# Optimization experiments

Hardware: AMD Instinct MI355X
Metric: run time of the kernel (lower is better)

Reference implementation:

```python
import jax, jax.numpy as jnp
import numpy as np
import math

N_HEAD = 16
HEAD_DIM = 64
LN_EPS = 1e-5
TEMP = 1.0

def _layernorm(x, scale, bias):
    # normalize over last dim (head_dim)
    mu = jnp.mean(x, axis=-1, keepdims=True)
    var = jnp.mean(jnp.square(x - mu), axis=-1, keepdims=True)
    return (x - mu) / jnp.sqrt(var + LN_EPS) * scale + bias

def setup_inputs() -> dict:
    key = jax.random.key(0)
    ks = jax.random.split(key, 3)
    B, S, C = 4, 2048, 1024
    x = jax.random.normal(ks[0], (B, S, C), dtype=jnp.float32)
    w_qkv = jax.random.normal(ks[1], (C, 3 * C), dtype=jnp.float32) * (C ** -0.5)
    w_proj = jax.random.normal(ks[2], (C, C), dtype=jnp.float32) * (C ** -0.5)
    return {
        "x": x,
        "w_qkv": w_qkv,
        "w_proj": w_proj,
        "q_scale": jnp.ones((HEAD_DIM,), jnp.float32),
        "q_bias": jnp.zeros((HEAD_DIM,), jnp.float32),
        "k_scale": jnp.ones((HEAD_DIM,), jnp.float32),
        "k_bias": jnp.zeros((HEAD_DIM,), jnp.float32),
    }

def reference(x, w_qkv, w_proj, q_scale, q_bias, k_scale, k_bias):
    B, S, C = x.shape
    H, D = N_HEAD, HEAD_DIM
    # qkv projection -> [B,S,3,H,D] -> [3,B,H,S,D]
    qkv = (x @ w_qkv).reshape(B, S, 3, H, D).transpose(2, 0, 3, 1, 4)
    q = _layernorm(qkv[0], q_scale, q_bias)
    k = _layernorm(qkv[1], k_scale, k_bias)
    v = qkv[2]
    # temperature-scaled logits, stable softmax
    inv = 1.0 / (math.sqrt(D) * max(TEMP, 1e-6))
    logits = jnp.einsum('bhqd,bhkd->bhqk', q, k) * inv
    att = jax.nn.softmax(logits, axis=-1)
    # entropy stats (track_stats=True path)
    s_raw = -jnp.sum(att * jnp.log(att + 1e-9), axis=-1)  # [B,H,S]
    batch_entropies = jnp.mean(s_raw / math.log(S), axis=(1, 2))  # [B]
    out = jnp.einsum('bhqk,bhkd->bhqd', att, v).transpose(0, 2, 1, 3).reshape(B, S, C)
    return out @ w_proj, batch_entropies
```

## Files before the change

### kernel.cpp

```cpp
#include <hip/hip_runtime.h>
#include <hip/hip_bf16.h>
#include <math.h>

#define CB 4
#define CS 2048
#define CC 1024
#define CH 16
#define CD 64
#define CBS (CB*CS)

typedef unsigned short u16;
typedef __bf16 bf16x8 __attribute__((ext_vector_type(8)));
typedef float f32x4 __attribute__((ext_vector_type(4)));
typedef float f32x16 __attribute__((ext_vector_type(16)));
typedef unsigned short u16x4 __attribute__((ext_vector_type(4)));
typedef unsigned short u16x8 __attribute__((ext_vector_type(8)));
typedef unsigned u32x2 __attribute__((ext_vector_type(2)));

__device__ __forceinline__ u16 f2bf(float f){
  union { float f; unsigned u; } v; v.f = f;
  unsigned r = v.u + 0x7FFFu + ((v.u >> 16) & 1u);
  return (u16)(r >> 16);
}
__device__ __forceinline__ unsigned pack2bf(float a, float b){
  __hip_bfloat162 h = __float22bfloat162_rn(make_float2(a, b));
  union { __hip_bfloat162 h; unsigned u; } c; c.h = h; return c.u;
}
__device__ __forceinline__ f32x4 mfma16(bf16x8 a, bf16x8 b, f32x4 c){
  return __builtin_amdgcn_mfma_f32_16x16x32_bf16(a, b, c, 0, 0, 0);
}
__device__ __forceinline__ f32x16 mfma32(bf16x8 a, bf16x8 b, f32x16 c){
  return __builtin_amdgcn_mfma_f32_32x32x16_bf16(a, b, c, 0, 0, 0);
}
__device__ __forceinline__ void gload16(const u16* g, u16* lds_base_uniform){
  __builtin_amdgcn_global_load_lds(
      (const __attribute__((address_space(1))) unsigned int*)g,
      (__attribute__((address_space(3))) unsigned int*)lds_base_uniform, 16, 0, 0);
}

__global__ __launch_bounds__(256) void convert_x_kernel(
    const float* __restrict__ x, u16* __restrict__ xb, float* __restrict__ zero4){
  if (blockIdx.x == 0 && threadIdx.x < 4) zero4[threadIdx.x] = 0.0f;
  size_t i = ((size_t)blockIdx.x*256 + threadIdx.x)*8;
  float4 a = *(const float4*)(x+i);
  float4 b = *(const float4*)(x+i+4);
  u16x8 o = { f2bf(a.x),f2bf(a.y),f2bf(a.z),f2bf(a.w),
              f2bf(b.x),f2bf(b.y),f2bf(b.z),f2bf(b.w) };
  *(u16x8*)(xb+i) = o;
}

template<int K, int N>
__global__ __launch_bounds__(256) void transpose_convert_kernel(
    const float* __restrict__ w, u16* __restrict__ wt){
  __shared__ u16 tile[64][65];
  const int nb = N/64;
  int tk0 = (blockIdx.x / nb) * 64;
  int tn0 = (blockIdx.x % nb) * 64;
  int t = threadIdx.x;
  for (int i = 0; i < 4; i++) {
    int r = i*16 + (t>>4);
    int c = (t&15)*4;
    float4 v = *(const float4*)(w + (size_t)(tk0+r)*N + tn0 + c);
    tile[c+0][r]=f2bf(v.x); tile[c+1][r]=f2bf(v.y);
    tile[c+2][r]=f2bf(v.z); tile[c+3][r]=f2bf(v.w);
  }
  __syncthreads();
  for (int i = 0; i < 4; i++) {
    int r = i*16 + (t>>4);
    int c = (t&15)*4;
    u16x4 o = { tile[r][c+0], tile[r][c+1], tile[r][c+2], tile[r][c+3] };
    *(u16x4*)(wt + (size_t)(tn0+r)*K + tk0 + c) = o;
  }
}

__global__ __launch_bounds__(256) void transpose_v_kernel(
    const u16* __restrict__ vb, u16* __restrict__ vtb){
  __shared__ u16 tile[64][72];
  int bh = blockIdx.x >> 5;
  int st = blockIdx.x & 31;
  int t = threadIdx.x;
  const u16* src = vb + (size_t)bh*CS*CD + (size_t)st*64*CD;
  int r = t>>2, c = (t&3)*16;
  *(u16x8*)&tile[r][c]   = *(const u16x8*)(src + (size_t)r*CD + c);
  *(u16x8*)&tile[r][c+8] = *(const u16x8*)(src + (size_t)r*CD + c + 8);
  __syncthreads();
  int d = t>>2, s = (t&3)*16;
  u16x8 o0, o1;
  for (int j=0;j<8;j++){ o0[j] = tile[s+j][d]; o1[j] = tile[s+8+j][d]; }
  u16* dst = vtb + (size_t)bh*CD*CS + (size_t)d*CS + st*64 + s;
  *(u16x8*)dst = o0;
  *(u16x8*)(dst+8) = o1;
}

__global__ __launch_bounds__(256, 2) void gemm_qkv_ln_kernel(
    const u16* __restrict__ xb, const u16* __restrict__ wqkvT,
    const float* __restrict__ qsc, const float* __restrict__ qbi,
    const float* __restrict__ ksc, const float* __restrict__ kbi,
    u16* __restrict__ qb, u16* __restrict__ kb, u16* __restrict__ vb){
  __shared__ u16 al[128*64];
  __shared__ u16 bl[128*64];
  int t = threadIdx.x;
  int wv = t >> 6, lane = t & 63, lo = lane & 15, q4 = lane >> 4;
  int m0 = blockIdx.x * 128;
  int n0 = blockIdx.y * 128;
  int srow = lane >> 3, scol = (lane & 7) * 8;
  const u16* ag = xb    + (size_t)(m0 + srow)*CC + scol;
  const u16* bg = wqkvT + (size_t)(n0 + srow)*CC + scol;

  f32x4 acc[2][8];
  for (int i=0;i<2;i++) for (int j=0;j<8;j++) acc[i][j] = (f32x4){0.f,0.f,0.f,0.f};

  for (int kk = 0; kk < 16; kk++){
    int k0 = kk * 64;
    for (int i = 0; i < 4; i++){
      int inst = i*4 + wv;
      gload16(ag + (size_t)inst*8*CC + k0, al + inst*512);
      gload16(bg + (size_t)inst*8*CC + k0, bl + inst*512);
    }
    __syncthreads();
    for (int ksI = 0; ksI < 2; ksI++){
      int koff = ksI*32 + q4*8;
      bf16x8 a0 = *(const bf16x8*)&al[(wv*32      + lo)*64 + koff];
      bf16x8 a1 = *(const bf16x8*)&al[(wv*32 + 16 + lo)*64 + koff];
      for (int nt=0; nt<8; nt++){
        bf16x8 b = *(const bf16x8*)&bl[(nt*16 + lo)*64 + koff];
        acc[0][nt] = mfma16(a0, b, acc[0][nt]);
        acc[1][nt] = mfma16(a1, b, acc[1][nt]);
      }
    }
    __syncthreads();
  }

  int three = n0 >> 10;
  int h0 = (n0 & 1023) >> 6;
  const float* scp = (three == 0) ? qsc : ksc;
  const float* bip = (three == 0) ? qbi : kbi;
  float outscale = (three == 0) ? 0.125f * 1.44269504088896f : 1.0f;
  u16* dst = (three == 0) ? qb : (three == 1 ? kb : vb);

  for (int rt = 0; rt < 2; rt++){
    int tg = m0 + wv*32 + rt*16 + q4*4;
    for (int hf = 0; hf < 2; hf++){
      int h = h0 + hf;
      for (int r = 0; r < 4; r++){
        int token = tg + r;
        int bb = token >> 11, ss = token & (CS-1);
        size_t base = (((size_t)(bb*CH + h))*CS + ss)*CD;
        if (three < 2){
          float s1 = 0.f, s2 = 0.f;
          for (int j=0;j<4;j++){ float v = acc[rt][hf*4+j][r]; s1 += v; s2 += v*v; }
          for (int off=8; off>=1; off>>=1){
            s1 += __shfl_xor(s1, off, 16);
            s2 += __shfl_xor(s2, off, 16);
          }
          float mean = s1 * (1.f/64.f);
          float var  = s2 * (1.f/64.f) - mean*mean;
          float rstd = rsqrtf(var + 1e-5f);
          for (int j=0;j<4;j++){
            int d = j*16 + lo;
            float v = (acc[rt][hf*4+j][r] - mean) * rstd * scp[d] + bip[d];
            dst[base + d] = f2bf(v * outscale);
          }
        } else {
          for (int j=0;j<4;j++){
            int d = j*16 + lo;
            dst[base + d] = f2bf(acc[rt][hf*4+j][r]);
          }
        }
      }
    }
  }
}

__global__ __launch_bounds__(256, 4) void attention_kernel(
    const u16* __restrict__ qb, const u16* __restrict__ kb,
    const u16* __restrict__ vtb, u16* __restrict__ attnb, float* __restrict__ ent){
  __shared__ __align__(16) u16 kl[2][64*64];
  __shared__ __align__(16) u16 vl[2][64*64];
  __shared__ __align__(16) float zl[4][32];
  int t = threadIdx.x;
  int wv = t >> 6, lane = t & 63;
  int col = lane & 31, hi = lane >> 5;
  int n = blockIdx.x;
  int xc = n & 7, j = n >> 3;
  int bh = xc + 8*(j >> 4);
  int qt = j & 15;
  int bI = bh >> 4;
  int q0w = qt*128 + wv*32;
  const u16* qbp = qb  + (size_t)bh * CS * CD;
  const u16* kbp = kb  + (size_t)bh * CS * CD;
  const u16* vbp = vtb + (size_t)bh * CD * CS;

  int srow  = lane >> 3;
  int sslot = (lane & 7) ^ srow;

  bf16x8 qf[4];
  for (int ks=0;ks<4;ks++)
    qf[ks] = *(const bf16x8*)(qbp + (size_t)(q0w + col)*CD + ks*16 + hi*8);

  f32x16 o[2];
  for (int nt=0;nt<2;nt++) for (int i=0;i<16;i++) o[nt][i] = 0.f;
  float zacc = 0.f, tacc = 0.f;

  for (int c=0;c<2;c++){
    int chunk = wv*2 + c;
    int row = chunk*8 + srow;
    gload16(kbp + (size_t)row*CD + sslot*8, &kl[0][chunk*512]);
    gload16(vbp + (size_t)row*CS + sslot*8, &vl[0][chunk*512]);
  }

  const int cshift = (col & 7);

  for (int it = 0; it < 32; it++){
    const int cur = it & 1, nxt = cur ^ 1;
    __syncthreads();
    if (it < 31){
      int skn = (it+1)*64;
      for (int c=0;c<2;c++){
        int chunk = wv*2 + c;
        int row = chunk*8 + srow;
        gload16(kbp + (size_t)(skn + row)*CD + sslot*8, &kl[nxt][chunk*512]);
        gload16(vbp + (size_t)row*CS + skn + sslot*8, &vl[nxt][chunk*512]);
      }
    }

    bf16x8 kfr[2][4], vfr[2][4];
    for (int mt=0;mt<2;mt++)
      for (int ks=0;ks<4;ks++)
        kfr[mt][ks] = *(const bf16x8*)&kl[cur][(mt*32+col)*64 + (((2*ks+hi)^cshift)<<3)];
    for (int nt=0;nt<2;nt++)
      for (int ks=0;ks<4;ks++)
        vfr[nt][ks] = *(const bf16x8*)&vl[cur][(nt*32+col)*64 + (((2*ks+hi)^cshift)<<3)];

    f32x16 sf[2];
    for (int mt=0;mt<2;mt++) for (int i=0;i<16;i++) sf[mt][i] = 0.f;
    for (int ks=0;ks<4;ks++){
      sf[0] = mfma32(kfr[0][ks], qf[ks], sf[0]);
      sf[1] = mfma32(kfr[1][ks], qf[ks], sf[1]);
    }

    for (int mt=0;mt<2;mt++){
      for (int ksl=0; ksl<2; ksl++){
        float p[2][4];
        for (int gg=0; gg<2; gg++){
          int g = 2*ksl + gg;
          float l0 = sf[mt][g*4+0], l1 = sf[mt][g*4+1],
                l2 = sf[mt][g*4+2], l3 = sf[mt][g*4+3];
          float p0 = __builtin_amdgcn_exp2f(l0);
          float p1 = __builtin_amdgcn_exp2f(l1);
          float p2 = __builtin_amdgcn_exp2f(l2);
          float p3 = __builtin_amdgcn_exp2f(l3);
          zacc += (p0+p1)+(p2+p3);
          tacc += (p0*l0+p1*l1)+(p2*l2+p3*l3);
          p[gg][0]=p0; p[gg][1]=p1; p[gg][2]=p2; p[gg][3]=p3;
        }
        unsigned x0 = pack2bf(p[0][0], p[0][1]);
        unsigned x1 = pack2bf(p[0][2], p[0][3]);
        unsigned y0 = pack2bf(p[1][0], p[1][1]);
        unsigned y1 = pack2bf(p[1][2], p[1][3]);
        u32x2 s0 = __builtin_amdgcn_permlane32_swap(x0, y0, false, false);
        u32x2 s1 = __builtin_amdgcn_permlane32_swap(x1, y1, false, false);
        union { unsigned u[4]; bf16x8 v; } ap;
        ap.u[0] = s0[0]; ap.u[1] = s1[0]; ap.u[2] = s0[1]; ap.u[3] = s1[1];
        int ks = mt*2 + ksl;
        o[0] = mfma32(ap.v, vfr[0][ks], o[0]);
        o[1] = mfma32(ap.v, vfr[1][ks], o[1]);
      }
    }
  }

  float z2 = zacc + __shfl_xor(zacc, 32);
  float t2 = tacc + __shfl_xor(tacc, 32);
  float invz = 1.f / z2;
  if (hi == 0) zl[wv][col] = invz;

  float srowv = 0.69314718055995f * (__builtin_amdgcn_logf(z2) - t2 * invz);
  float ev = (hi == 0) ? srowv : 0.f;
  for (int off=1; off<=32; off<<=1) ev += __shfl_xor(ev, off);
  if (lane == 0){
    float entscale = 1.0f / ((float)CH * (float)CS * logf((float)CS));
    atomicAdd(&ent[bI], ev * entscale);
  }

  u16* obase = attnb + ((size_t)bh*CS + q0w)*CD;
  for (int nt=0;nt<2;nt++){
    for (int g=0;g<4;g++){
      f32x4 iz = *(const f32x4*)&zl[wv][g*8 + hi*4];
      for (int r=0;r<4;r++){
        int qrow = 8*g + 4*hi + r;
        obase[(size_t)qrow*CD + nt*32 + col] = f2bf(o[nt][g*4+r] * iz[r]);
      }
    }
  }
}

__global__ __launch_bounds__(256, 2) void gemm_out_kernel(
    const u16* __restrict__ attnH, const u16* __restrict__ wprojT,
    float* __restrict__ out){
  __shared__ u16 al[128*64];
  __shared__ u16 bl[128*64];
  int t = threadIdx.x;
  int wv = t >> 6, lane = t & 63, lo = lane & 15, q4 = lane >> 4;
  int m0 = blockIdx.x * 128;
  int n0 = blockIdx.y * 128;
  int b  = m0 >> 11, s0 = m0 & (CS-1);
  int srow = lane >> 3, scol = (lane & 7) * 8;
  const u16* bg = wprojT + (size_t)(n0 + srow)*CC + scol;

  f32x4 acc[2][8];
  for (int i=0;i<2;i++) for (int j=0;j<8;j++) acc[i][j] = (f32x4){0.f,0.f,0.f,0.f};

  for (int kk = 0; kk < 16; kk++){
    const u16* abase = attnH + ((size_t)(b*CH + kk)*CS + s0 + srow)*CD + scol;
    for (int i = 0; i < 4; i++){
      int inst = i*4 + wv;
      gload16(abase + (size_t)inst*8*CD, al + inst*512);
      gload16(bg + (size_t)inst*8*CC + kk*64, bl + inst*512);
    }
    __syncthreads();
    for (int ksI = 0; ksI < 2; ksI++){
      int koff = ksI*32 + q4*8;
      bf16x8 a0 = *(const bf16x8*)&al[(wv*32      + lo)*64 + koff];
      bf16x8 a1 = *(const bf16x8*)&al[(wv*32 + 16 + lo)*64 + koff];
      for (int nt=0; nt<8; nt++){
        bf16x8 b2 = *(const bf16x8*)&bl[(nt*16 + lo)*64 + koff];
        acc[0][nt] = mfma16(a0, b2, acc[0][nt]);
        acc[1][nt] = mfma16(a1, b2, acc[1][nt]);
      }
    }
    __syncthreads();
  }

  for (int rt=0;rt<2;rt++){
    for (int r=0;r<4;r++){
      int row = m0 + wv*32 + rt*16 + q4*4 + r;
      for (int nt=0;nt<8;nt++)
        out[(size_t)row*CC + n0 + nt*16 + lo] = acc[rt][nt][r];
    }
  }
}

extern "C" void kernel_launch(void* const* d_in, const int* in_sizes, int n_in,
                              void* d_out, int out_size, void* d_ws, size_t ws_size,
                              hipStream_t stream) {
  const float* x      = (const float*)d_in[0];
  const float* w_qkv  = (const float*)d_in[1];
  const float* w_proj = (const float*)d_in[2];
  const float* q_scale= (const float*)d_in[3];
  const float* q_bias = (const float*)d_in[4];
  const float* k_scale= (const float*)d_in[5];
  const float* k_bias = (const float*)d_in[6];
  float* out = (float*)d_out;
  float* ent = out + (size_t)CBS * CC;

  u16* xb     = (u16*)d_ws;
  u16* wqkvT  = xb     + (size_t)CBS*CC;
  u16* wprojT = wqkvT  + (size_t)3*CC*CC;
  u16* qb     = wprojT + (size_t)CC*CC;
  u16* kb     = qb + (size_t)CB*CH*CS*CD;
  u16* vb     = kb + (size_t)CB*CH*CS*CD;
  u16* vbT    = xb;
  u16* attn   = vb;

  convert_x_kernel<<<dim3(CBS*CC/(256*8)), 256, 0, stream>>>(x, xb, ent);
  transpose_convert_kernel<CC, 3*CC><<<dim3((CC/64)*(3*CC/64)), 256, 0, stream>>>(w_qkv, wqkvT);
  transpose_convert_kernel<CC, CC><<<dim3((CC/64)*(CC/64)), 256, 0, stream>>>(w_proj, wprojT);
  gemm_qkv_ln_kernel<<<dim3(CBS/128, 3*CC/128), 256, 0, stream>>>(
      xb, wqkvT, q_scale, q_bias, k_scale, k_bias, qb, kb, vb);
  transpose_v_kernel<<<dim3(CB*CH*(CS/64)), 256, 0, stream>>>(vb, vbT);
  attention_kernel<<<dim3(CB*CH*(CS/128)), 256, 0, stream>>>(qb, kb, vbT, attn, ent);
  gemm_out_kernel<<<dim3(CBS/128, CC/128), 256, 0, stream>>>(attn, wprojT, out);
}
```

Measured before the change: 359.0 us.

## Tune attention kernel occupancy, LDS swizzle, MFMA priority and shuffle-based normalization

Raises the attention kernel's launch-bounds occupancy hint from 4 to 5 blocks per CU. It also changes the LDS XOR swizzle to include the chunk and row-group bits, which is meant to reduce bank conflicts. The MFMA blocks are wrapped in s_setprio, loops get explicit unroll pragmas, and the shared-memory 1/z buffer is replaced by wave shuffles. The higher occupancy target may force register spills, and the shuffle broadcast adds cross-lane operations in place of an LDS round trip.

```diff
diff --git a/kernel.cpp b/kernel.cpp
--- a/kernel.cpp
+++ b/kernel.cpp
@@ -172,12 +172,11 @@
   }
 }
 
-__global__ __launch_bounds__(256, 4) void attention_kernel(
+__global__ __launch_bounds__(256, 5) void attention_kernel(
     const u16* __restrict__ qb, const u16* __restrict__ kb,
     const u16* __restrict__ vtb, u16* __restrict__ attnb, float* __restrict__ ent){
   __shared__ __align__(16) u16 kl[2][64*64];
   __shared__ __align__(16) u16 vl[2][64*64];
-  __shared__ __align__(16) float zl[4][32];
   int t = threadIdx.x;
   int wv = t >> 6, lane = t & 63;
   int col = lane & 31, hi = lane >> 5;
@@ -191,57 +190,78 @@
   const u16* kbp = kb  + (size_t)bh * CS * CD;
   const u16* vbp = vtb + (size_t)bh * CD * CS;
 
-  int srow  = lane >> 3;
-  int sslot = (lane & 7) ^ srow;
+  int srow = lane >> 3;
+  int sl   = lane & 7;
 
   bf16x8 qf[4];
+  #pragma unroll
   for (int ks=0;ks<4;ks++)
     qf[ks] = *(const bf16x8*)(qbp + (size_t)(q0w + col)*CD + ks*16 + hi*8);
 
   f32x16 o[2];
-  for (int nt=0;nt<2;nt++) for (int i=0;i<16;i++) o[nt][i] = 0.f;
+  #pragma unroll
+  for (int nt=0;nt<2;nt++)
+    #pragma unroll
+    for (int i=0;i<16;i++) o[nt][i] = 0.f;
   float zacc = 0.f, tacc = 0.f;
 
+  #pragma unroll
   for (int c=0;c<2;c++){
     int chunk = wv*2 + c;
-    int row = chunk*8 + srow;
-    gload16(kbp + (size_t)row*CD + sslot*8, &kl[0][chunk*512]);
-    gload16(vbp + (size_t)row*CS + sslot*8, &vl[0][chunk*512]);
-  }
-
-  const int cshift = (col & 7);
+    int slot  = sl ^ srow ^ chunk;
+    int row   = chunk*8 + srow;
+    gload16(kbp + (size_t)row*CD + slot*8, &kl[0][chunk*512]);
+    gload16(vbp + (size_t)row*CS + slot*8, &vl[0][chunk*512]);
+  }
+
+  const int ckey = (col & 7) ^ (col >> 3);
 
   for (int it = 0; it < 32; it++){
     const int cur = it & 1, nxt = cur ^ 1;
     __syncthreads();
     if (it < 31){
       int skn = (it+1)*64;
+      #pragma unroll
       for (int c=0;c<2;c++){
         int chunk = wv*2 + c;
-        int row = chunk*8 + srow;
-        gload16(kbp + (size_t)(skn + row)*CD + sslot*8, &kl[nxt][chunk*512]);
-        gload16(vbp + (size_t)row*CS + skn + sslot*8, &vl[nxt][chunk*512]);
+        int slot  = sl ^ srow ^ chunk;
+        int row   = chunk*8 + srow;
+        gload16(kbp + (size_t)(skn + row)*CD + slot*8, &kl[nxt][chunk*512]);
+        gload16(vbp + (size_t)row*CS + skn + slot*8, &vl[nxt][chunk*512]);
       }
     }
 
     bf16x8 kfr[2][4], vfr[2][4];
+    #pragma unroll
     for (int mt=0;mt<2;mt++)
+      #pragma unroll
       for (int ks=0;ks<4;ks++)
-        kfr[mt][ks] = *(const bf16x8*)&kl[cur][(mt*32+col)*64 + (((2*ks+hi)^cshift)<<3)];
+        kfr[mt][ks] = *(const bf16x8*)&kl[cur][(mt*32+col)*64 + (((2*ks+hi) ^ ckey ^ (mt<<2))<<3)];
+    #pragma unroll
     for (int nt=0;nt<2;nt++)
+      #pragma unroll
       for (int ks=0;ks<4;ks++)
-        vfr[nt][ks] = *(const bf16x8*)&vl[cur][(nt*32+col)*64 + (((2*ks+hi)^cshift)<<3)];
+        vfr[nt][ks] = *(const bf16x8*)&vl[cur][(nt*32+col)*64 + (((2*ks+hi) ^ ckey ^ (nt<<2))<<3)];
 
     f32x16 sf[2];
-    for (int mt=0;mt<2;mt++) for (int i=0;i<16;i++) sf[mt][i] = 0.f;
+    #pragma unroll
+    for (int mt=0;mt<2;mt++)
+      #pragma unroll
+      for (int i=0;i<16;i++) sf[mt][i] = 0.f;
+    __builtin_amdgcn_s_setprio(1);
+    #pragma unroll
     for (int ks=0;ks<4;ks++){
       sf[0] = mfma32(kfr[0][ks], qf[ks], sf[0]);
       sf[1] = mfma32(kfr[1][ks], qf[ks], sf[1]);
     }
-
+    __builtin_amdgcn_s_setprio(0);
+
+    #pragma unroll
     for (int mt=0;mt<2;mt++){
+      #pragma unroll
       for (int ksl=0; ksl<2; ksl++){
         float p[2][4];
+        #pragma unroll
         for (int gg=0; gg<2; gg++){
           int g = 2*ksl + gg;
           float l0 = sf[mt][g*4+0], l1 = sf[mt][g*4+1],
@@ -263,8 +283,10 @@
         union { unsigned u[4]; bf16x8 v; } ap;
         ap.u[0] = s0[0]; ap.u[1] = s1[0]; ap.u[2] = s0[1]; ap.u[3] = s1[1];
         int ks = mt*2 + ksl;
+        __builtin_amdgcn_s_setprio(1);
         o[0] = mfma32(ap.v, vfr[0][ks], o[0]);
         o[1] = mfma32(ap.v, vfr[1][ks], o[1]);
+        __builtin_amdgcn_s_setprio(0);
       }
     }
   }
@@ -272,7 +294,6 @@
   float z2 = zacc + __shfl_xor(zacc, 32);
   float t2 = tacc + __shfl_xor(tacc, 32);
   float invz = 1.f / z2;
-  if (hi == 0) zl[wv][col] = invz;
 
   float srowv = 0.69314718055995f * (__builtin_amdgcn_logf(z2) - t2 * invz);
   float ev = (hi == 0) ? srowv : 0.f;
@@ -282,13 +303,22 @@
     atomicAdd(&ent[bI], ev * entscale);
   }
 
+  float izv[4][4];
+  #pragma unroll
+  for (int g=0; g<4; g++)
+    #pragma unroll
+    for (int r=0; r<4; r++)
+      izv[g][r] = __shfl(invz, 8*g + 4*hi + r);
+
   u16* obase = attnb + ((size_t)bh*CS + q0w)*CD;
+  #pragma unroll
   for (int nt=0;nt<2;nt++){
+    #pragma unroll
     for (int g=0;g<4;g++){
-      f32x4 iz = *(const f32x4*)&zl[wv][g*8 + hi*4];
+      #pragma unroll
       for (int r=0;r<4;r++){
         int qrow = 8*g + 4*hi + r;
-        obase[(size_t)qrow*CD + nt*32 + col] = f2bf(o[nt][g*4+r] * iz[r]);
+        obase[(size_t)qrow*CD + nt*32 + col] = f2bf(o[nt][g*4+r] * izv[g][r]);
       }
     }
   }
```

Result: slower. 1.248 ms (+247.7%).
